# Kernel tuning notes

Measured on AMD Instinct MI355X. Metric: run time of the kernel, lower is better.

## Reference

```python
import jax, jax.numpy as jnp
import numpy as np

B, L, S, D, V, H = 8, 1024, 1024, 256, 256, 8
HD = D // H   # traj head dim = 32
VD = V // H   # value head dim = 32
SCALE = HD ** -0.5

def _xavier(key, shape):
    fan_in, fan_out = shape[1], shape[0]
    std = (2.0 / (fan_in + fan_out)) ** 0.5
    return jax.random.normal(key, shape, dtype=jnp.float32) * std

def setup_inputs() -> dict:
    key = jax.random.key(0)
    ks = jax.random.split(key, 12)
    return {
        "q": jax.random.normal(ks[0], (B, L, D), dtype=jnp.float32),
        "k": jax.random.normal(ks[1], (B, S, D), dtype=jnp.float32),
        "v": jax.random.normal(ks[2], (B, S, D), dtype=jnp.float32),
        "q_identities": jax.random.randint(ks[3], (B, L), 0, 16),
        "k_identities": jax.random.randint(ks[4], (B, S), 0, 16),
        "mask": jnp.zeros((B, L, S), dtype=jnp.float32),
        "w_q_self": _xavier(ks[5], (D, D)),
        "w_q_other": _xavier(ks[6], (D, D)),
        "w_k_self": _xavier(ks[7], (D, D)),
        "w_k_other": _xavier(ks[8], (D, D)),
        "w_v": _xavier(ks[9], (V, D)),
        "fc_w": _xavier(ks[10], (V, V)),
        "fc_b": jnp.zeros((V,), dtype=jnp.float32),
    }

def _heads(x, hd):
    # [B, T, H*hd] -> [B, H, T, hd]
    Bc, T, _ = x.shape
    return x.reshape(Bc, T, H, hd).transpose(0, 2, 1, 3)

def reference(q, k, v, q_identities, k_identities, mask,
              w_q_self, w_q_other, w_k_self, w_k_other, w_v, fc_w, fc_b):
    # torch Linear: y = x @ W.T
    q_self = _heads(q @ w_q_self.T, HD) * SCALE   # [B,H,L,hd]
    q_other = _heads(q @ w_q_other.T, HD) * SCALE
    k_self = _heads(k @ w_k_self.T, HD)           # [B,H,S,hd]
    k_other = _heads(k @ w_k_other.T, HD)
    vh = _heads(v @ w_v.T, VD)                    # [B,H,S,vd]

    att_self = jnp.einsum('bhld,bhsd->bhls', q_self, k_self)
    att_other = jnp.einsum('bhld,bhsd->bhls', q_other, k_other)

    same = (q_identities[:, :, None] == k_identities[:, None, :])[:, None]  # [B,1,L,S]
    attention = jnp.where(same, att_self, att_other) + mask[:, None]
    attention = jax.nn.softmax(attention, axis=-1)  # [B,H,L,S]

    out = jnp.einsum('bhls,bhsd->bhld', attention, vh)     # [B,H,L,vd]
    out = out.transpose(0, 2, 1, 3).reshape(B, L, V)
    out = out @ fc_w.T + fc_b
    return out, attention.sum(axis=1) / H
```

## Files before the change

### kernel.cpp

```cpp
#include <hip/hip_runtime.h>
#include <hip/hip_bf16.h>

typedef float f32x4 __attribute__((ext_vector_type(4)));
typedef __bf16 bf16x8 __attribute__((ext_vector_type(8)));
typedef unsigned short us4 __attribute__((ext_vector_type(4)));

constexpr int B = 8, L = 1024, S = 1024, H = 8;
constexpr float LOG2E = 1.4426950408889634f;
constexpr float SCALE_Q = 0.17677669529663687f * 1.4426950408889634f;

__device__ __forceinline__ unsigned short bfbits(float x) {
  return __builtin_bit_cast(unsigned short, (__bf16)x);
}
__device__ __forceinline__ float b2f(unsigned short u) {
  return __builtin_bit_cast(float, (unsigned int)u << 16);
}

__global__ __launch_bounds__(256) void prep_mask_kernel(
    const float* __restrict__ mask, __bf16* __restrict__ maskT)
{
  __shared__ float tile[16][65];
  const int tid = threadIdx.x;
  const int sc = blockIdx.x, lt = blockIdx.y, b = blockIdx.z;
  const int s0 = sc * 64;
  const int q = tid >> 6, sl = tid & 63;
  #pragma unroll
  for (int rr = 0; rr < 4; ++rr) {
    int row = q * 4 + rr;
    tile[row][sl] = mask[((size_t)(b * 1024 + lt * 16 + row)) * 1024 + s0 + sl] * LOG2E;
  }
  __syncthreads();
  const int sl2 = tid >> 2, rq = (tid & 3) * 4;
  us4 o;
  #pragma unroll
  for (int j = 0; j < 4; ++j) o[j] = bfbits(tile[rq + j][sl2]);
  *reinterpret_cast<us4*>(maskT + (((size_t)(b * 64 + lt)) * 1024 + s0 + sl2) * 16 + rq) = o;
}

__global__ __launch_bounds__(256) void proj_kernel(
    const float* __restrict__ q, const float* __restrict__ k, const float* __restrict__ v,
    const float* __restrict__ wqs, const float* __restrict__ wqo,
    const float* __restrict__ wks, const float* __restrict__ wko,
    const float* __restrict__ wv,
    __bf16* __restrict__ qs, __bf16* __restrict__ qo,
    __bf16* __restrict__ ksl, __bf16* __restrict__ kol,
    __bf16* __restrict__ vht)
{
  const int proj = blockIdx.z;
  const float* X; const float* W;
  if (proj == 0)      { X = q; W = wqs; }
  else if (proj == 1) { X = q; W = wqo; }
  else if (proj == 2) { X = k; W = wks; }
  else if (proj == 3) { X = k; W = wko; }
  else                { X = v; W = wv;  }

  __shared__ __align__(16) char smem[2 * 64 * 264 * 2];
  __bf16 (*At)[264] = (__bf16(*)[264])smem;
  __bf16 (*Wt)[264] = (__bf16(*)[264])(smem + 64 * 264 * 2);
  float  (*ct)[65]  = (float(*)[65])smem;

  const int tid = threadIdx.x;
  const int m0 = blockIdx.y * 64, n0 = blockIdx.x * 64;

  for (int i = tid; i < 4096; i += 256) {
    int row = i >> 6, c4 = (i & 63) << 2;
    float4 a  = *reinterpret_cast<const float4*>(X + (size_t)(m0 + row) * 256 + c4);
    float4 ww = *reinterpret_cast<const float4*>(W + (size_t)(n0 + row) * 256 + c4);
    us4 ap, wp;
    ap[0] = bfbits(a.x);  ap[1] = bfbits(a.y);  ap[2] = bfbits(a.z);  ap[3] = bfbits(a.w);
    wp[0] = bfbits(ww.x); wp[1] = bfbits(ww.y); wp[2] = bfbits(ww.z); wp[3] = bfbits(ww.w);
    *reinterpret_cast<us4*>(&At[row][c4]) = ap;
    *reinterpret_cast<us4*>(&Wt[row][c4]) = wp;
  }
  __syncthreads();

  const int w = tid >> 6, lane = tid & 63;
  const int cl = lane & 15, g = lane >> 4;

  f32x4 zf = {0.f, 0.f, 0.f, 0.f};
  f32x4 acc[4] = {zf, zf, zf, zf};
  #pragma unroll
  for (int kk = 0; kk < 8; ++kk) {
    bf16x8 af = *reinterpret_cast<const bf16x8*>(&At[w * 16 + cl][kk * 32 + g * 8]);
    #pragma unroll
    for (int nt = 0; nt < 4; ++nt) {
      bf16x8 bfr = *reinterpret_cast<const bf16x8*>(&Wt[nt * 16 + cl][kk * 32 + g * 8]);
      acc[nt] = __builtin_amdgcn_mfma_f32_16x16x32_bf16(af, bfr, acc[nt], 0, 0, 0);
    }
  }
  if (proj < 2) {
    #pragma unroll
    for (int nt = 0; nt < 4; ++nt)
      #pragma unroll
      for (int r = 0; r < 4; ++r) acc[nt][r] *= SCALE_Q;
  }

  if (proj < 4) {
    __bf16* Y = (proj == 0) ? qs : (proj == 1) ? qo : (proj == 2) ? ksl : kol;
    #pragma unroll
    for (int nt = 0; nt < 4; ++nt) {
      int n = n0 + nt * 16 + cl;
      int h = n >> 5, hd = n & 31;
      #pragma unroll
      for (int r = 0; r < 4; ++r) {
        int m = m0 + w * 16 + g * 4 + r;
        int bb = m >> 10, t = m & 1023;
        Y[(((size_t)(bb * H + h)) * 1024 + t) * 32 + hd] = (__bf16)acc[nt][r];
      }
    }
  } else {
    __syncthreads();
    #pragma unroll
    for (int nt = 0; nt < 4; ++nt)
      #pragma unroll
      for (int r = 0; r < 4; ++r)
        ct[w * 16 + g * 4 + r][nt * 16 + cl] = acc[nt][r];
    __syncthreads();
    int n_local = tid >> 2;
    int sc = (tid & 3) << 4;
    int n = n0 + n_local;
    int h = n >> 5, vd = n & 31;
    int bb = m0 >> 10;
    int sbase = m0 & 1023;
    int t32 = (sbase + sc) >> 5, off = (sbase + sc) & 31;
    __bf16* dst = vht + ((((size_t)(bb * H + h)) * 32 + t32)) * 1024 + vd * 32 + off;
    bf16x8 o0, o1;
    #pragma unroll
    for (int j = 0; j < 8; ++j) o0[j] = (__bf16)ct[sc + j][n_local];
    #pragma unroll
    for (int j = 0; j < 8; ++j) o1[j] = (__bf16)ct[sc + 8 + j][n_local];
    *reinterpret_cast<bf16x8*>(dst) = o0;
    *reinterpret_cast<bf16x8*>(dst + 8) = o1;
  }
}

__global__ __launch_bounds__(256) void attn_kernel(
    const __bf16* __restrict__ qs, const __bf16* __restrict__ qo,
    const __bf16* __restrict__ ksl, const __bf16* __restrict__ kol,
    const __bf16* __restrict__ vht,
    const int* __restrict__ qid, const int* __restrict__ kid,
    const __bf16* __restrict__ maskT,
    float* __restrict__ out_part, __bf16* __restrict__ att_part)
{
  const int b = blockIdx.y;
  const int lt = blockIdx.x;
  const int l0 = lt * 16;
  const int hg = blockIdx.z;
  const int tid = threadIdx.x;
  const int w = tid >> 6, lane = tid & 63;
  const int cl = lane & 15, g = lane >> 4;
  const int sw = w * 256;

  __shared__ __align__(16) __bf16 pbuf[4][16][264];
  __shared__ float redsum[2][4][16];

  int qid_r[4];
  #pragma unroll
  for (int r = 0; r < 4; ++r) qid_r[r] = qid[b * L + l0 + g * 4 + r];
  int kid_st[16];
  #pragma unroll
  for (int st = 0; st < 16; ++st) kid_st[st] = kid[b * S + sw + st * 16 + cl];

  us4 mreg[16];
  {
    const __bf16* mbase = maskT + ((size_t)(b * 64 + lt)) * 16384 + (size_t)(sw + cl) * 16 + g * 4;
    #pragma unroll
    for (int st = 0; st < 16; ++st)
      mreg[st] = *reinterpret_cast<const us4*>(mbase + st * 256);
  }

  f32x4 zf = {0.f, 0.f, 0.f, 0.f};
  float att_acc[8][8];
  #pragma unroll
  for (int kt = 0; kt < 8; ++kt)
    #pragma unroll
    for (int j = 0; j < 8; ++j) att_acc[kt][j] = 0.f;

  const size_t PSZ = (size_t)B * L * 256;

  for (int hi = 0; hi < 2; ++hi) {
    const int h = hg * 2 + hi;
    const int par = hi;
    const size_t hb = ((size_t)(b * H + h)) * 1024;

    bf16x8 qsf = *reinterpret_cast<const bf16x8*>(qs + (hb + l0 + cl) * 32 + g * 8);
    bf16x8 qof = *reinterpret_cast<const bf16x8*>(qo + (hb + l0 + cl) * 32 + g * 8);
    const __bf16* kb1 = ksl + (hb + sw) * 32;
    const __bf16* kb2 = kol + (hb + sw) * 32;

    float rsum[4] = {0.f, 0.f, 0.f, 0.f};
    #pragma unroll
    for (int st = 0; st < 16; ++st) {
      bf16x8 kf1 = *reinterpret_cast<const bf16x8*>(kb1 + st * 512 + cl * 32 + g * 8);
      bf16x8 kf2 = *reinterpret_cast<const bf16x8*>(kb2 + st * 512 + cl * 32 + g * 8);
      f32x4 as = __builtin_amdgcn_mfma_f32_16x16x32_bf16(qsf, kf1, zf, 0, 0, 0);
      f32x4 ao = __builtin_amdgcn_mfma_f32_16x16x32_bf16(qof, kf2, zf, 0, 0, 0);
      int kc = kid_st[st];
      #pragma unroll
      for (int r = 0; r < 4; ++r) {
        float lg = ((qid_r[r] == kc) ? as[r] : ao[r]) + b2f(mreg[st][r]);
        float p = __builtin_amdgcn_exp2f(fminf(lg, 86.0f));
        pbuf[w][g * 4 + r][st * 16 + cl] = (__bf16)p;
        rsum[r] += p;
      }
    }

    #pragma unroll
    for (int r = 0; r < 4; ++r) {
      float sv = rsum[r];
      sv += __shfl_xor(sv, 1); sv += __shfl_xor(sv, 2);
      sv += __shfl_xor(sv, 4); sv += __shfl_xor(sv, 8);
      rsum[r] = sv;
    }
    if (cl == 0) {
      #pragma unroll
      for (int r = 0; r < 4; ++r) redsum[par][w][g * 4 + r] = rsum[r];
    }
    __syncthreads();
    float zrow = redsum[par][0][cl] + redsum[par][1][cl] +
                 redsum[par][2][cl] + redsum[par][3][cl];
    float inv_cl = 1.0f / zrow;
    float invq[4];
    #pragma unroll
    for (int r = 0; r < 4; ++r) invq[r] = __shfl(inv_cl, g * 4 + r);

    f32x4 oa0 = zf, oa1 = zf;
    const __bf16* vb = vht + ((size_t)(b * H + h)) * 32 * 1024 + (size_t)w * 8 * 1024;
    #pragma unroll
    for (int kt = 0; kt < 8; ++kt) {
      bf16x8 pa = *reinterpret_cast<const bf16x8*>(&pbuf[w][cl][kt * 32 + g * 8]);
      #pragma unroll
      for (int j = 0; j < 8; ++j) att_acc[kt][j] += (float)pa[j] * inv_cl;
      bf16x8 v0 = *reinterpret_cast<const bf16x8*>(vb + kt * 1024 + cl * 32 + g * 8);
      bf16x8 v1 = *reinterpret_cast<const bf16x8*>(vb + kt * 1024 + 512 + cl * 32 + g * 8);
      oa0 = __builtin_amdgcn_mfma_f32_16x16x32_bf16(pa, v0, oa0, 0, 0, 0);
      oa1 = __builtin_amdgcn_mfma_f32_16x16x32_bf16(pa, v1, oa1, 0, 0, 0);
    }
    float* op = out_part + (size_t)w * PSZ + ((size_t)(b * 1024 + l0)) * 256 + h * 32;
    #pragma unroll
    for (int r = 0; r < 4; ++r) {
      op[(size_t)(g * 4 + r) * 256 + cl]      = oa0[r] * invq[r];
      op[(size_t)(g * 4 + r) * 256 + cl + 16] = oa1[r] * invq[r];
    }
  }

  __bf16* ap = att_part + (size_t)hg * ((size_t)B * L * S) +
               ((size_t)(b * 1024 + l0 + cl)) * 1024 + sw + g * 8;
  #pragma unroll
  for (int kt = 0; kt < 8; ++kt) {
    bf16x8 o;
    #pragma unroll
    for (int j = 0; j < 8; ++j) o[j] = (__bf16)(att_acc[kt][j] * 0.125f);
    *reinterpret_cast<bf16x8*>(ap + kt * 32) = o;
  }
}

__global__ __launch_bounds__(256) void fc_kernel(
    const float* __restrict__ part, const float* __restrict__ fcw,
    const float* __restrict__ fcb, float* __restrict__ out)
{
  __shared__ __align__(16) __bf16 At[64][264];
  __shared__ __align__(16) __bf16 Wt[64][264];
  const int tid = threadIdx.x;
  const int m0 = blockIdx.y * 64, n0 = blockIdx.x * 64;
  const size_t PSZ = (size_t)B * L * 256;

  for (int i = tid; i < 4096; i += 256) {
    int row = i >> 6, c4 = (i & 63) << 2;
    size_t off = (size_t)(m0 + row) * 256 + c4;
    float4 s0 = *reinterpret_cast<const float4*>(part + off);
    float4 s1 = *reinterpret_cast<const float4*>(part + PSZ + off);
    float4 s2 = *reinterpret_cast<const float4*>(part + 2 * PSZ + off);
    float4 s3 = *reinterpret_cast<const float4*>(part + 3 * PSZ + off);
    float4 ww = *reinterpret_cast<const float4*>(fcw + (size_t)(n0 + row) * 256 + c4);
    us4 ap, wp;
    ap[0] = bfbits(s0.x + s1.x + s2.x + s3.x);
    ap[1] = bfbits(s0.y + s1.y + s2.y + s3.y);
    ap[2] = bfbits(s0.z + s1.z + s2.z + s3.z);
    ap[3] = bfbits(s0.w + s1.w + s2.w + s3.w);
    wp[0] = bfbits(ww.x); wp[1] = bfbits(ww.y); wp[2] = bfbits(ww.z); wp[3] = bfbits(ww.w);
    *reinterpret_cast<us4*>(&At[row][c4]) = ap;
    *reinterpret_cast<us4*>(&Wt[row][c4]) = wp;
  }
  __syncthreads();

  const int w = tid >> 6, lane = tid & 63;
  const int cl = lane & 15, g = lane >> 4;
  f32x4 zf = {0.f, 0.f, 0.f, 0.f};
  f32x4 acc[4] = {zf, zf, zf, zf};
  #pragma unroll
  for (int kk = 0; kk < 8; ++kk) {
    bf16x8 af = *reinterpret_cast<const bf16x8*>(&At[w * 16 + cl][kk * 32 + g * 8]);
    #pragma unroll
    for (int nt = 0; nt < 4; ++nt) {
      bf16x8 bfr = *reinterpret_cast<const bf16x8*>(&Wt[nt * 16 + cl][kk * 32 + g * 8]);
      acc[nt] = __builtin_amdgcn_mfma_f32_16x16x32_bf16(af, bfr, acc[nt], 0, 0, 0);
    }
  }
  #pragma unroll
  for (int nt = 0; nt < 4; ++nt) {
    int n = n0 + nt * 16 + cl;
    float bias = fcb[n];
    #pragma unroll
    for (int r = 0; r < 4; ++r)
      out[(size_t)(m0 + w * 16 + g * 4 + r) * 256 + n] = acc[nt][r] + bias;
  }
}

__global__ __launch_bounds__(256) void reduce_att_kernel(
    const __bf16* __restrict__ ap, float* __restrict__ am)
{
  const size_t APSZ = (size_t)B * L * S;
  size_t i = ((size_t)blockIdx.x * 256 + threadIdx.x) * 8;
  bf16x8 a = *reinterpret_cast<const bf16x8*>(ap + i);
  bf16x8 c = *reinterpret_cast<const bf16x8*>(ap + APSZ + i);
  bf16x8 d = *reinterpret_cast<const bf16x8*>(ap + 2 * APSZ + i);
  bf16x8 e = *reinterpret_cast<const bf16x8*>(ap + 3 * APSZ + i);
  float4 o0, o1;
  o0.x = ((float)a[0] + (float)c[0]) + ((float)d[0] + (float)e[0]);
  o0.y = ((float)a[1] + (float)c[1]) + ((float)d[1] + (float)e[1]);
  o0.z = ((float)a[2] + (float)c[2]) + ((float)d[2] + (float)e[2]);
  o0.w = ((float)a[3] + (float)c[3]) + ((float)d[3] + (float)e[3]);
  o1.x = ((float)a[4] + (float)c[4]) + ((float)d[4] + (float)e[4]);
  o1.y = ((float)a[5] + (float)c[5]) + ((float)d[5] + (float)e[5]);
  o1.z = ((float)a[6] + (float)c[6]) + ((float)d[6] + (float)e[6]);
  o1.w = ((float)a[7] + (float)c[7]) + ((float)d[7] + (float)e[7]);
  *reinterpret_cast<float4*>(am + i) = o0;
  *reinterpret_cast<float4*>(am + i + 4) = o1;
}

extern "C" void kernel_launch(void* const* d_in, const int* in_sizes, int n_in,
                              void* d_out, int out_size, void* d_ws, size_t ws_size,
                              hipStream_t stream) {
  const float* q    = (const float*)d_in[0];
  const float* k    = (const float*)d_in[1];
  const float* v    = (const float*)d_in[2];
  const int*   qid  = (const int*)d_in[3];
  const int*   kid  = (const int*)d_in[4];
  const float* mask = (const float*)d_in[5];
  const float* wqs  = (const float*)d_in[6];
  const float* wqo  = (const float*)d_in[7];
  const float* wks  = (const float*)d_in[8];
  const float* wko  = (const float*)d_in[9];
  const float* wv   = (const float*)d_in[10];
  const float* fcw  = (const float*)d_in[11];
  const float* fcb  = (const float*)d_in[12];

  char* ws = (char*)d_ws;
  const size_t ACT  = (size_t)B * L * 256 * sizeof(__bf16);
  const size_t PSZB = (size_t)B * L * 256 * sizeof(float);
  const size_t APSZB = (size_t)B * L * S * sizeof(__bf16);
  __bf16* qs  = (__bf16*)(ws + 0 * ACT);
  __bf16* qo  = (__bf16*)(ws + 1 * ACT);
  __bf16* ksl = (__bf16*)(ws + 2 * ACT);
  __bf16* kol = (__bf16*)(ws + 3 * ACT);
  __bf16* vht = (__bf16*)(ws + 4 * ACT);
  float*  out_part = (float*)(ws + 5 * ACT);
  __bf16* att_part = (__bf16*)(ws + 5 * ACT + 4 * PSZB);
  __bf16* maskT    = (__bf16*)(ws + 5 * ACT + 4 * PSZB + 4 * APSZB);

  float* out0 = (float*)d_out;
  float* att_mean = out0 + (size_t)B * L * 256;

  prep_mask_kernel<<<dim3(16, 64, 8), 256, 0, stream>>>(mask, maskT);
  proj_kernel<<<dim3(4, 128, 5), 256, 0, stream>>>(q, k, v, wqs, wqo, wks, wko, wv,
                                                   qs, qo, ksl, kol, vht);
  attn_kernel<<<dim3(64, 8, 4), 256, 0, stream>>>(qs, qo, ksl, kol, vht, qid, kid, maskT,
                                                  out_part, att_part);
  fc_kernel<<<dim3(4, 128), 256, 0, stream>>>(out_part, fcw, fcb, out0);
  reduce_att_kernel<<<dim3(4096), 256, 0, stream>>>(att_part, att_mean);
}
```

Baseline: 288.8 us.

## Process all heads per block and write head-mean attention directly, dropping reduce kernel

The attention kernel now runs 512 threads (8 waves, each covering 128 keys) and loops over all 8 heads inside one block, instead of splitting heads into 4 groups across blocks. Because every head is handled in one block, the head-averaged attention is accumulated in registers and written straight to the fp32 output. This removes the bf16 partial attention buffers and the separate reduce kernel, cutting a large amount of global memory traffic. The cost is 8 output partials that the FC kernel must now sum instead of 4, a smaller grid (512 blocks), and a longer serial head loop per block.

```diff
diff --git a/kernel.cpp b/kernel.cpp
--- a/kernel.cpp
+++ b/kernel.cpp
@@ -134,53 +134,51 @@
   }
 }
 
-__global__ __launch_bounds__(256) void attn_kernel(
+__global__ __launch_bounds__(512, 4) void attn_kernel(
     const __bf16* __restrict__ qs, const __bf16* __restrict__ qo,
     const __bf16* __restrict__ ksl, const __bf16* __restrict__ kol,
     const __bf16* __restrict__ vht,
     const int* __restrict__ qid, const int* __restrict__ kid,
     const __bf16* __restrict__ maskT,
-    float* __restrict__ out_part, __bf16* __restrict__ att_part)
+    float* __restrict__ out_part, float* __restrict__ att_mean)
 {
   const int b = blockIdx.y;
   const int lt = blockIdx.x;
   const int l0 = lt * 16;
-  const int hg = blockIdx.z;
   const int tid = threadIdx.x;
   const int w = tid >> 6, lane = tid & 63;
   const int cl = lane & 15, g = lane >> 4;
-  const int sw = w * 256;
-
-  __shared__ __align__(16) __bf16 pbuf[4][16][264];
-  __shared__ float redsum[2][4][16];
+  const int sw = w * 128;
+
+  __shared__ __align__(16) __bf16 pbuf[8][16][140];
+  __shared__ float redsum[2][8][16];
 
   int qid_r[4];
   #pragma unroll
   for (int r = 0; r < 4; ++r) qid_r[r] = qid[b * L + l0 + g * 4 + r];
-  int kid_st[16];
-  #pragma unroll
-  for (int st = 0; st < 16; ++st) kid_st[st] = kid[b * S + sw + st * 16 + cl];
-
-  us4 mreg[16];
+  int kid_st[8];
+  #pragma unroll
+  for (int st = 0; st < 8; ++st) kid_st[st] = kid[b * S + sw + st * 16 + cl];
+
+  us4 mreg[8];
   {
     const __bf16* mbase = maskT + ((size_t)(b * 64 + lt)) * 16384 + (size_t)(sw + cl) * 16 + g * 4;
     #pragma unroll
-    for (int st = 0; st < 16; ++st)
+    for (int st = 0; st < 8; ++st)
       mreg[st] = *reinterpret_cast<const us4*>(mbase + st * 256);
   }
 
   f32x4 zf = {0.f, 0.f, 0.f, 0.f};
-  float att_acc[8][8];
-  #pragma unroll
-  for (int kt = 0; kt < 8; ++kt)
+  float att_acc[4][8];
+  #pragma unroll
+  for (int kt = 0; kt < 4; ++kt)
     #pragma unroll
     for (int j = 0; j < 8; ++j) att_acc[kt][j] = 0.f;
 
   const size_t PSZ = (size_t)B * L * 256;
 
-  for (int hi = 0; hi < 2; ++hi) {
-    const int h = hg * 2 + hi;
-    const int par = hi;
+  for (int h = 0; h < H; ++h) {
+    const int par = h & 1;
     const size_t hb = ((size_t)(b * H + h)) * 1024;
 
     bf16x8 qsf = *reinterpret_cast<const bf16x8*>(qs + (hb + l0 + cl) * 32 + g * 8);
@@ -190,7 +188,7 @@
 
     float rsum[4] = {0.f, 0.f, 0.f, 0.f};
     #pragma unroll
-    for (int st = 0; st < 16; ++st) {
+    for (int st = 0; st < 8; ++st) {
       bf16x8 kf1 = *reinterpret_cast<const bf16x8*>(kb1 + st * 512 + cl * 32 + g * 8);
       bf16x8 kf2 = *reinterpret_cast<const bf16x8*>(kb2 + st * 512 + cl * 32 + g * 8);
       f32x4 as = __builtin_amdgcn_mfma_f32_16x16x32_bf16(qsf, kf1, zf, 0, 0, 0);
@@ -217,17 +215,18 @@
       for (int r = 0; r < 4; ++r) redsum[par][w][g * 4 + r] = rsum[r];
     }
     __syncthreads();
-    float zrow = redsum[par][0][cl] + redsum[par][1][cl] +
-                 redsum[par][2][cl] + redsum[par][3][cl];
+    float zrow = 0.f;
+    #pragma unroll
+    for (int q8 = 0; q8 < 8; ++q8) zrow += redsum[par][q8][cl];
     float inv_cl = 1.0f / zrow;
     float invq[4];
     #pragma unroll
     for (int r = 0; r < 4; ++r) invq[r] = __shfl(inv_cl, g * 4 + r);
 
     f32x4 oa0 = zf, oa1 = zf;
-    const __bf16* vb = vht + ((size_t)(b * H + h)) * 32 * 1024 + (size_t)w * 8 * 1024;
-    #pragma unroll
-    for (int kt = 0; kt < 8; ++kt) {
+    const __bf16* vb = vht + ((size_t)(b * H + h)) * 32 * 1024 + (size_t)w * 4 * 1024;
+    #pragma unroll
+    for (int kt = 0; kt < 4; ++kt) {
       bf16x8 pa = *reinterpret_cast<const bf16x8*>(&pbuf[w][cl][kt * 32 + g * 8]);
       #pragma unroll
       for (int j = 0; j < 8; ++j) att_acc[kt][j] += (float)pa[j] * inv_cl;
@@ -244,14 +243,16 @@
     }
   }
 
-  __bf16* ap = att_part + (size_t)hg * ((size_t)B * L * S) +
-               ((size_t)(b * 1024 + l0 + cl)) * 1024 + sw + g * 8;
-  #pragma unroll
-  for (int kt = 0; kt < 8; ++kt) {
-    bf16x8 o;
-    #pragma unroll
-    for (int j = 0; j < 8; ++j) o[j] = (__bf16)(att_acc[kt][j] * 0.125f);
-    *reinterpret_cast<bf16x8*>(ap + kt * 32) = o;
+  float* am = att_mean + ((size_t)(b * 1024 + l0 + cl)) * 1024 + sw + g * 8;
+  #pragma unroll
+  for (int kt = 0; kt < 4; ++kt) {
+    float4 o0, o1;
+    o0.x = att_acc[kt][0] * 0.125f; o0.y = att_acc[kt][1] * 0.125f;
+    o0.z = att_acc[kt][2] * 0.125f; o0.w = att_acc[kt][3] * 0.125f;
+    o1.x = att_acc[kt][4] * 0.125f; o1.y = att_acc[kt][5] * 0.125f;
+    o1.z = att_acc[kt][6] * 0.125f; o1.w = att_acc[kt][7] * 0.125f;
+    *reinterpret_cast<float4*>(am + kt * 32) = o0;
+    *reinterpret_cast<float4*>(am + kt * 32 + 4) = o1;
   }
 }
 
@@ -269,15 +270,14 @@
     int row = i >> 6, c4 = (i & 63) << 2;
     size_t off = (size_t)(m0 + row) * 256 + c4;
     float4 s0 = *reinterpret_cast<const float4*>(part + off);
-    float4 s1 = *reinterpret_cast<const float4*>(part + PSZ + off);
-    float4 s2 = *reinterpret_cast<const float4*>(part + 2 * PSZ + off);
-    float4 s3 = *reinterpret_cast<const float4*>(part + 3 * PSZ + off);
+    #pragma unroll
+    for (int p = 1; p < 8; ++p) {
+      float4 sp = *reinterpret_cast<const float4*>(part + (size_t)p * PSZ + off);
+      s0.x += sp.x; s0.y += sp.y; s0.z += sp.z; s0.w += sp.w;
+    }
     float4 ww = *reinterpret_cast<const float4*>(fcw + (size_t)(n0 + row) * 256 + c4);
     us4 ap, wp;
-    ap[0] = bfbits(s0.x + s1.x + s2.x + s3.x);
-    ap[1] = bfbits(s0.y + s1.y + s2.y + s3.y);
-    ap[2] = bfbits(s0.z + s1.z + s2.z + s3.z);
-    ap[3] = bfbits(s0.w + s1.w + s2.w + s3.w);
+    ap[0] = bfbits(s0.x); ap[1] = bfbits(s0.y); ap[2] = bfbits(s0.z); ap[3] = bfbits(s0.w);
     wp[0] = bfbits(ww.x); wp[1] = bfbits(ww.y); wp[2] = bfbits(ww.z); wp[3] = bfbits(ww.w);
     *reinterpret_cast<us4*>(&At[row][c4]) = ap;
     *reinterpret_cast<us4*>(&Wt[row][c4]) = wp;
@@ -305,28 +305,6 @@
     for (int r = 0; r < 4; ++r)
       out[(size_t)(m0 + w * 16 + g * 4 + r) * 256 + n] = acc[nt][r] + bias;
   }
-}
-
-__global__ __launch_bounds__(256) void reduce_att_kernel(
-    const __bf16* __restrict__ ap, float* __restrict__ am)
-{
-  const size_t APSZ = (size_t)B * L * S;
-  size_t i = ((size_t)blockIdx.x * 256 + threadIdx.x) * 8;
-  bf16x8 a = *reinterpret_cast<const bf16x8*>(ap + i);
-  bf16x8 c = *reinterpret_cast<const bf16x8*>(ap + APSZ + i);
-  bf16x8 d = *reinterpret_cast<const bf16x8*>(ap + 2 * APSZ + i);
-  bf16x8 e = *reinterpret_cast<const bf16x8*>(ap + 3 * APSZ + i);
-  float4 o0, o1;
-  o0.x = ((float)a[0] + (float)c[0]) + ((float)d[0] + (float)e[0]);
-  o0.y = ((float)a[1] + (float)c[1]) + ((float)d[1] + (float)e[1]);
-  o0.z = ((float)a[2] + (float)c[2]) + ((float)d[2] + (float)e[2]);
-  o0.w = ((float)a[3] + (float)c[3]) + ((float)d[3] + (float)e[3]);
-  o1.x = ((float)a[4] + (float)c[4]) + ((float)d[4] + (float)e[4]);
-  o1.y = ((float)a[5] + (float)c[5]) + ((float)d[5] + (float)e[5]);
-  o1.z = ((float)a[6] + (float)c[6]) + ((float)d[6] + (float)e[6]);
-  o1.w = ((float)a[7] + (float)c[7]) + ((float)d[7] + (float)e[7]);
-  *reinterpret_cast<float4*>(am + i) = o0;
-  *reinterpret_cast<float4*>(am + i + 4) = o1;
 }
 
 extern "C" void kernel_launch(void* const* d_in, const int* in_sizes, int n_in,
@@ -349,15 +327,13 @@
   char* ws = (char*)d_ws;
   const size_t ACT  = (size_t)B * L * 256 * sizeof(__bf16);
   const size_t PSZB = (size_t)B * L * 256 * sizeof(float);
-  const size_t APSZB = (size_t)B * L * S * sizeof(__bf16);
   __bf16* qs  = (__bf16*)(ws + 0 * ACT);
   __bf16* qo  = (__bf16*)(ws + 1 * ACT);
   __bf16* ksl = (__bf16*)(ws + 2 * ACT);
   __bf16* kol = (__bf16*)(ws + 3 * ACT);
   __bf16* vht = (__bf16*)(ws + 4 * ACT);
   float*  out_part = (float*)(ws + 5 * ACT);
-  __bf16* att_part = (__bf16*)(ws + 5 * ACT + 4 * PSZB);
-  __bf16* maskT    = (__bf16*)(ws + 5 * ACT + 4 * PSZB + 4 * APSZB);
+  __bf16* maskT    = (__bf16*)(ws + 5 * ACT + 8 * PSZB);
 
   float* out0 = (float*)d_out;
   float* att_mean = out0 + (size_t)B * L * 256;
@@ -365,8 +341,7 @@
   prep_mask_kernel<<<dim3(16, 64, 8), 256, 0, stream>>>(mask, maskT);
   proj_kernel<<<dim3(4, 128, 5), 256, 0, stream>>>(q, k, v, wqs, wqo, wks, wko, wv,
                                                    qs, qo, ksl, kol, vht);
-  attn_kernel<<<dim3(64, 8, 4), 256, 0, stream>>>(qs, qo, ksl, kol, vht, qid, kid, maskT,
-                                                  out_part, att_part);
+  attn_kernel<<<dim3(64, 8), 512, 0, stream>>>(qs, qo, ksl, kol, vht, qid, kid, maskT,
+                                               out_part, att_mean);
   fc_kernel<<<dim3(4, 128), 256, 0, stream>>>(out_part, fcw, fcb, out0);
-  reduce_att_kernel<<<dim3(4096), 256, 0, stream>>>(att_part, att_mean);
-}
+}
```

After: 282.3 us. -2.3%, faster.
